# Kernel tuning notes

Measured on AMD Instinct MI355X. Metric: run time of the kernel, lower is better.

## Reference

```python
import jax, jax.numpy as jnp
import numpy as np

S = 2048      # total tokens
DIM = 1024    # model dim
H = 16        # attention heads
DH = 64       # head dim
BOT = 256     # bottleneck dim
NIMG = 4      # images (equal size)
L = S // NIMG # tokens per image
K = 256       # sparse_k
IH = 4        # indexer heads
ID = 16       # indexer head dim
MAXREL = 64   # hardcoded in module
NBUCK = 2 * MAXREL + 1
GH = IH * 2   # gate MLP hidden (expansion=2)


def setup_inputs() -> dict:
    key = jax.random.key(0)
    ks = jax.random.split(key, 16)
    r = lambda i, sh, s=0.02: jax.random.normal(ks[i], sh, jnp.float32) * s
    return dict(
        hidden_states=jax.random.normal(ks[0], (S, DIM), jnp.float32),
        patch_coords=jax.random.randint(ks[1], (S, 2), 0, 64, dtype=jnp.int32),
        cu_seqlens=jnp.arange(NIMG + 1, dtype=jnp.int32) * L,
        rotary_pos_emb=jax.random.uniform(ks[2], (S, DH // 2), jnp.float32) * 3.0,
        Wq_idx=r(3, (2 * IH * ID, DIM)),
        Wk_idx=r(4, (2 * IH * ID, DIM)),
        W1g=r(5, (GH, IH)), b1g=jnp.zeros((GH,), jnp.float32),
        W2g=r(6, (IH, GH)), b2g=jnp.zeros((IH,), jnp.float32),
        rpe_table=r(7, (NBUCK, IH)),
        Wqkv_d=r(8, (BOT, DIM)), bqkv_d=jnp.zeros((BOT,), jnp.float32),
        Wqkv_u=r(9, (3 * DIM, BOT)), bqkv_u=jnp.zeros((3 * DIM,), jnp.float32),
        Wp_d=r(10, (BOT, DIM)), bp_d=jnp.zeros((BOT,), jnp.float32),
        Wp_u=r(11, (DIM, BOT)), bp_u=jnp.zeros((DIM,), jnp.float32),
        scaler=jnp.ones((1,), jnp.float32),
    )


def _rotate_half(x):
    x1, x2 = jnp.split(x, 2, axis=-1)
    return jnp.concatenate([-x2, x1], axis=-1)


def reference(hidden_states, patch_coords, cu_seqlens, rotary_pos_emb,
              Wq_idx, Wk_idx, W1g, b1g, W2g, b2g, rpe_table,
              Wqkv_d, bqkv_d, Wqkv_u, bqkv_u, Wp_d, bp_d, Wp_u, bp_u, scaler):
    n = cu_seqlens.shape[0] - 1            # images (equal size L)
    Li = hidden_states.shape[0] // n
    neg = jnp.finfo(hidden_states.dtype).min

    # QKV via low-rank bottleneck
    qkv = (hidden_states @ Wqkv_d.T + bqkv_d) @ Wqkv_u.T + bqkv_u  # [S, 3*DIM]
    qkv = qkv.reshape(S, 3, H, DH)
    q, k, v = qkv[:, 0], qkv[:, 1], qkv[:, 2]                      # [S, H, DH]

    # vision RoPE (emb = cat(rpe, rpe))
    emb = jnp.concatenate([rotary_pos_emb, rotary_pos_emb], axis=-1)  # [S, DH]
    cos = jnp.cos(emb)[:, None, :]
    sin = jnpp if False else jnp.sin(emb)[:, None, :]
    q = q * cos + _rotate_half(q) * sin
    k = k * cos + _rotate_half(k) * sin

    # ---- interaction indexer, vmapped over equal-size images ----
    xs = hidden_states.reshape(n, Li, DIM)
    pos = patch_coords[:, 1].reshape(n, Li).astype(jnp.float32)
    qI = (xs @ Wq_idx.T).reshape(n, Li, 2 * IH, ID)
    kI = (xs @ Wk_idx.T).reshape(n, Li, 2 * IH, ID)
    dot = jnp.einsum('nqhd,nkhd->nqkh', qI, kI)                    # [n, L, L, 2*IH]
    data_in, gate_in = dot[..., :IH], dot[..., IH:]
    rel = jnp.clip(pos[:, :, None] - pos[:, None, :], -MAXREL, MAXREL)
    bucket = (rel + MAXREL).astype(jnp.int32)                      # [n, L, L]
    rpe = rpe_table[bucket]                                        # [n, L, L, IH]
    relu_scores = jax.nn.relu(data_in + rpe)
    g = jax.nn.sigmoid(jax.nn.relu((gate_in + rpe) @ W1g.T + b1g) @ W2g.T + b2g)
    index_scores = (relu_scores * g).sum(-1)                       # [n, L, L]

    # top-k sparse mask (0 at selected keys, -inf-ish elsewhere)
    _, topk_idx = jax.lax.top_k(index_scores, K)                   # [n, L, K]
    ni = jnp.arange(n)[:, None, None]
    ri = jnp.arange(Li)[None, :, None]
    mask_local = jnp.full((n, Li, Li), neg, hidden_states.dtype).at[ni, ri, topk_idx].set(0.0)

    # block-diagonal full mask
    mask = jnp.full((S, S), neg, hidden_states.dtype)
    for i in range(n):
        mask = mask.at[i * Li:(i + 1) * Li, i * Li:(i + 1) * Li].set(mask_local[i])

    # dense SDPA with additive mask
    att = jnp.einsum('qhd,khd->hqk', q, k) / jnp.sqrt(jnp.float32(DH)).astype(q.dtype)
    att = att + mask[None]
    p = jax.nn.softmax(att, axis=-1)
    out = jnp.einsum('hqk,khd->qhd', p, v).reshape(S, H * DH)

    final = (out @ Wp_d.T + bp_d) @ Wp_u.T + bp_u
    return final * scaler
```

## Files before the change

kernel.cpp:

```cpp
#include <hip/hip_runtime.h>
#include <hip/hip_bf16.h>

#define S_    2048
#define DIM_  1024
#define H_    16
#define DH_   64
#define BOT_  256
#define NIMG_ 4
#define LI_   512
#define K_    256
#define IH_   4
#define ID_   16
#define MAXREL_ 64
#define NBUCK_ 129
#define GH_   8
#define IDH2_ 128

typedef short bf16x8 __attribute__((ext_vector_type(8)));
typedef float f32x4  __attribute__((ext_vector_type(4)));

__device__ __forceinline__ unsigned short f2bf(float x) {
    unsigned u = __float_as_uint(x);
    return (unsigned short)((u + 0x7fffu + ((u >> 16) & 1u)) >> 16);
}
__device__ __forceinline__ float bf2f(unsigned short h) {
    return __uint_as_float(((unsigned)h) << 16);
}

#define OFF_W1_    2097152
#define OFF_WQ_    2359296
#define OFF_WK_    2490368
#define OFF_WQKVU_ 2621440
#define OFF_WPD_   3407872
#define OFF_WPU_   3670016
#define NSPLIT_    3932160

__global__ __launch_bounds__(256) void split_all_kernel(
    const float* __restrict__ hid, const float* __restrict__ wqd,
    const float* __restrict__ wq,  const float* __restrict__ wk,
    const float* __restrict__ wqu, const float* __restrict__ wpd,
    const float* __restrict__ wpu,
    unsigned short* __restrict__ hi, unsigned short* __restrict__ lo)
{
    long e = ((long)blockIdx.x * 256 + threadIdx.x) * 4;
    if (e >= NSPLIT_) return;
    const float* src; long off;
    if (e < OFF_W1_)         { src = hid; off = 0; }
    else if (e < OFF_WQ_)    { src = wqd; off = OFF_W1_; }
    else if (e < OFF_WK_)    { src = wq;  off = OFF_WQ_; }
    else if (e < OFF_WQKVU_) { src = wk;  off = OFF_WK_; }
    else if (e < OFF_WPD_)   { src = wqu; off = OFF_WQKVU_; }
    else if (e < OFF_WPU_)   { src = wpd; off = OFF_WPD_; }
    else                     { src = wpu; off = OFF_WPU_; }
    float4 v = *(const float4*)(src + (e - off));
    ushort4 h, l;
    h.x = f2bf(v.x); l.x = f2bf(v.x - bf2f(h.x));
    h.y = f2bf(v.y); l.y = f2bf(v.y - bf2f(h.y));
    h.z = f2bf(v.z); l.z = f2bf(v.z - bf2f(h.z));
    h.w = f2bf(v.w); l.w = f2bf(v.w - bf2f(h.w));
    *(ushort4*)&hi[e] = h;
    *(ushort4*)&lo[e] = l;
}

__global__ __launch_bounds__(256) void gemm_bf16x3(
    const unsigned short* __restrict__ Ah, const unsigned short* __restrict__ Al,
    const unsigned short* __restrict__ Bh, const unsigned short* __restrict__ Bl,
    const float* __restrict__ bias, const float* __restrict__ scale_ptr,
    float* __restrict__ Cf, int M, int N, int Kd)
{
    __shared__ unsigned short sAh[128 * 40], sAl[128 * 40];
    __shared__ unsigned short sBh[64 * 40],  sBl[64 * 40];
    int tid = threadIdx.x;
    int lane = tid & 63, wv = tid >> 6;
    int wr = wv >> 1, wc = wv & 1;
    int row0 = blockIdx.y * 128, col0 = blockIdx.x * 64;

    f32x4 acc[4][2];
#pragma unroll
    for (int i = 0; i < 4; i++)
#pragma unroll
        for (int j = 0; j < 2; j++) acc[i][j] = (f32x4){0.f, 0.f, 0.f, 0.f};

    int ar = tid >> 1, ac = (tid & 1) * 16;
    int br = tid >> 2, bc = (tid & 3) * 8;
    const unsigned short* gAh = Ah + (size_t)(row0 + ar) * Kd + ac;
    const unsigned short* gAl = Al + (size_t)(row0 + ar) * Kd + ac;
    const unsigned short* gBh = Bh + (size_t)(col0 + br) * Kd + bc;
    const unsigned short* gBl = Bl + (size_t)(col0 + br) * Kd + bc;
    int am = lane & 15, qk = (lane >> 4) * 8;

    for (int k0 = 0; k0 < Kd; k0 += 32) {
        __syncthreads();
        *(float4*)&sAh[ar * 40 + ac]     = *(const float4*)(gAh + k0);
        *(float4*)&sAh[ar * 40 + ac + 8] = *(const float4*)(gAh + k0 + 8);
        *(float4*)&sAl[ar * 40 + ac]     = *(const float4*)(gAl + k0);
        *(float4*)&sAl[ar * 40 + ac + 8] = *(const float4*)(gAl + k0 + 8);
        *(float4*)&sBh[br * 40 + bc]     = *(const float4*)(gBh + k0);
        *(float4*)&sBl[br * 40 + bc]     = *(const float4*)(gBl + k0);
        __syncthreads();

        bf16x8 ah[4], al[4], bh[2], bl[2];
#pragma unroll
        for (int rt = 0; rt < 4; rt++) {
            int r = wr * 64 + rt * 16 + am;
            ah[rt] = *(const bf16x8*)&sAh[r * 40 + qk];
            al[rt] = *(const bf16x8*)&sAl[r * 40 + qk];
        }
#pragma unroll
        for (int ct = 0; ct < 2; ct++) {
            int c = wc * 32 + ct * 16 + am;
            bh[ct] = *(const bf16x8*)&sBh[c * 40 + qk];
            bl[ct] = *(const bf16x8*)&sBl[c * 40 + qk];
        }
#pragma unroll
        for (int rt = 0; rt < 4; rt++)
#pragma unroll
            for (int ct = 0; ct < 2; ct++) {
                acc[rt][ct] = __builtin_amdgcn_mfma_f32_16x16x32_bf16(ah[rt], bh[ct], acc[rt][ct], 0, 0, 0);
                acc[rt][ct] = __builtin_amdgcn_mfma_f32_16x16x32_bf16(ah[rt], bl[ct], acc[rt][ct], 0, 0, 0);
                acc[rt][ct] = __builtin_amdgcn_mfma_f32_16x16x32_bf16(al[rt], bh[ct], acc[rt][ct], 0, 0, 0);
            }
    }

    float scl = scale_ptr ? *scale_ptr : 1.0f;
    int rq = (lane >> 4) * 4;
#pragma unroll
    for (int rt = 0; rt < 4; rt++)
#pragma unroll
        for (int ct = 0; ct < 2; ct++) {
            int col = col0 + wc * 32 + ct * 16 + am;
            float bz = bias ? bias[col] : 0.0f;
#pragma unroll
            for (int rg = 0; rg < 4; rg++) {
                int row = row0 + wr * 64 + rt * 16 + rq + rg;
                Cf[(size_t)row * N + col] = (acc[rt][ct][rg] + bz) * scl;
            }
        }
}

__global__ __launch_bounds__(256) void gemm64_bf16x3(
    const unsigned short* __restrict__ Ah, const unsigned short* __restrict__ Al,
    const unsigned short* __restrict__ Bh, const unsigned short* __restrict__ Bl,
    const float* __restrict__ bias_lo, const float* __restrict__ bias_hi,
    float* __restrict__ Cf, unsigned short* __restrict__ Chi,
    unsigned short* __restrict__ Clo, int M, int N, int Kd, int split_col)
{
    __shared__ unsigned short sAh[64 * 40], sAl[64 * 40];
    __shared__ unsigned short sBh[64 * 40], sBl[64 * 40];
    int tid = threadIdx.x;
    int lane = tid & 63, wv = tid >> 6;
    int wr = wv >> 1, wc = wv & 1;
    int row0 = blockIdx.y * 64, col0 = blockIdx.x * 64;

    f32x4 acc[2][2];
#pragma unroll
    for (int i = 0; i < 2; i++)
#pragma unroll
        for (int j = 0; j < 2; j++) acc[i][j] = (f32x4){0.f, 0.f, 0.f, 0.f};

    int sr = tid >> 2, sc = (tid & 3) * 8;
    const unsigned short* gAh = Ah + (size_t)(row0 + sr) * Kd + sc;
    const unsigned short* gAl = Al + (size_t)(row0 + sr) * Kd + sc;
    const unsigned short* gBh = Bh + (size_t)(col0 + sr) * Kd + sc;
    const unsigned short* gBl = Bl + (size_t)(col0 + sr) * Kd + sc;
    int am = lane & 15, qk = (lane >> 4) * 8;

    for (int k0 = 0; k0 < Kd; k0 += 32) {
        __syncthreads();
        *(float4*)&sAh[sr * 40 + sc] = *(const float4*)(gAh + k0);
        *(float4*)&sAl[sr * 40 + sc] = *(const float4*)(gAl + k0);
        *(float4*)&sBh[sr * 40 + sc] = *(const float4*)(gBh + k0);
        *(float4*)&sBl[sr * 40 + sc] = *(const float4*)(gBl + k0);
        __syncthreads();

        bf16x8 ah[2], al[2], bh[2], bl[2];
#pragma unroll
        for (int rt = 0; rt < 2; rt++) {
            int r = wr * 32 + rt * 16 + am;
            ah[rt] = *(const bf16x8*)&sAh[r * 40 + qk];
            al[rt] = *(const bf16x8*)&sAl[r * 40 + qk];
        }
#pragma unroll
        for (int ct = 0; ct < 2; ct++) {
            int c = wc * 32 + ct * 16 + am;
            bh[ct] = *(const bf16x8*)&sBh[c * 40 + qk];
            bl[ct] = *(const bf16x8*)&sBl[c * 40 + qk];
        }
#pragma unroll
        for (int rt = 0; rt < 2; rt++)
#pragma unroll
            for (int ct = 0; ct < 2; ct++) {
                acc[rt][ct] = __builtin_amdgcn_mfma_f32_16x16x32_bf16(ah[rt], bh[ct], acc[rt][ct], 0, 0, 0);
                acc[rt][ct] = __builtin_amdgcn_mfma_f32_16x16x32_bf16(ah[rt], bl[ct], acc[rt][ct], 0, 0, 0);
                acc[rt][ct] = __builtin_amdgcn_mfma_f32_16x16x32_bf16(al[rt], bh[ct], acc[rt][ct], 0, 0, 0);
            }
    }

    int rq = (lane >> 4) * 4;
#pragma unroll
    for (int rt = 0; rt < 2; rt++)
#pragma unroll
        for (int ct = 0; ct < 2; ct++) {
            int col = col0 + wc * 32 + ct * 16 + am;
#pragma unroll
            for (int rg = 0; rg < 4; rg++) {
                int row = row0 + wr * 32 + rt * 16 + rq + rg;
                float v = acc[rt][ct][rg];
                if (col < split_col) {
                    if (bias_lo) v += bias_lo[col];
                    size_t idx = (size_t)row * split_col + col;
                    unsigned short hh = f2bf(v);
                    Chi[idx] = hh;
                    Clo[idx] = f2bf(v - bf2f(hh));
                } else {
                    if (bias_hi) v += bias_hi[col - split_col];
                    Cf[(size_t)row * (N - split_col) + col - split_col] = v;
                }
            }
        }
}

__global__ __launch_bounds__(256) void rope_kernel(
    float* __restrict__ qkv, const float* __restrict__ rope)
{
    int idx = blockIdx.x * blockDim.x + threadIdx.x;
    if (idx >= S_ * H_ * 32) return;
    int d = idx & 31;
    int h = (idx >> 5) & (H_ - 1);
    int s = idx >> 9;
    float r = rope[s * 32 + d];
    float c = cosf(r), sn = sinf(r);
    size_t base = (size_t)s * 3072 + h * 64 + d;
    float q1 = qkv[base], q2 = qkv[base + 32];
    qkv[base]      = q1 * c - q2 * sn;
    qkv[base + 32] = q2 * c + q1 * sn;
    float k1 = qkv[base + 1024], k2 = qkv[base + 1024 + 32];
    qkv[base + 1024]      = k1 * c - k2 * sn;
    qkv[base + 1024 + 32] = k2 * c + k1 * sn;
}

__global__ __launch_bounds__(256) void score_topk_kernel(
    const float* __restrict__ qIk,
    const int* __restrict__ coords, const float* __restrict__ rpe_table,
    const float* __restrict__ W1g, const float* __restrict__ b1g,
    const float* __restrict__ W2g, const float* __restrict__ b2g,
    unsigned* __restrict__ selmask)
{
    __shared__ float skI[64][132];
    __shared__ float sqI2[4][IDH2_];
    __shared__ unsigned skeys[4][LI_];
    __shared__ int shist[4][256];
    __shared__ float srpe[NBUCK_ * IH_];
    __shared__ float sW1[GH_ * IH_], sb1[GH_], sW2[IH_ * GH_], sb2[IH_];

    int tid  = threadIdx.x;
    int lane = tid & 63;
    int wv   = tid >> 6;
    int row  = blockIdx.x * 4 + wv;
    int n    = (blockIdx.x * 4) >> 9;

    for (int i = tid; i < NBUCK_ * IH_; i += 256) srpe[i] = rpe_table[i];
    if (tid < 32) sW1[tid] = W1g[tid];
    else if (tid < 64) sW2[tid - 32] = W2g[tid - 32];
    else if (tid < 72) sb1[tid - 64] = b1g[tid - 64];
    else if (tid < 76) sb2[tid - 72] = b2g[tid - 72];
    for (int i = tid; i < 4 * IDH2_; i += 256)
        sqI2[i >> 7][i & 127] =
            qIk[(size_t)(blockIdx.x * 4 + (i >> 7)) * 256 + (i & 127)];
    int pq = coords[row * 2 + 1];

    for (int kt = 0; kt < 8; kt++) {
        __syncthreads();
        {
            int r  = tid >> 2;
            int d0 = (tid & 3) * 32;
            const float* src = qIk + (size_t)(n * LI_ + kt * 64 + r) * 256 + 128 + d0;
#pragma unroll
            for (int j = 0; j < 8; j++)
                *(float4*)&skI[r][d0 + j * 4] = *(const float4*)(src + j * 4);
        }
        __syncthreads();

        int kloc = lane;
        int kg   = kt * 64 + kloc;
        const float* sq = &sqI2[wv][0];
        float dh[8];
#pragma unroll
        for (int hh = 0; hh < 8; hh++) {
            float acc = 0.0f;
#pragma unroll
            for (int d = 0; d < 16; d += 4) {
                float4 kv = *(const float4*)&skI[kloc][hh * 16 + d];
                acc += sq[hh * 16 + d + 0] * kv.x + sq[hh * 16 + d + 1] * kv.y +
                       sq[hh * 16 + d + 2] * kv.z + sq[hh * 16 + d + 3] * kv.w;
            }
            dh[hh] = acc;
        }
        int pk = coords[(n * LI_ + kg) * 2 + 1];
        int rel = pq - pk;
        rel = rel < -MAXREL_ ? -MAXREL_ : (rel > MAXREL_ ? MAXREL_ : rel);
        const float* rp = srpe + (rel + MAXREL_) * IH_;
        float t1[GH_];
#pragma unroll
        for (int g = 0; g < GH_; g++) t1[g] = sb1[g];
#pragma unroll
        for (int j = 0; j < IH_; j++) {
            float gate = dh[IH_ + j] + rp[j];
#pragma unroll
            for (int g = 0; g < GH_; g++) t1[g] += gate * sW1[g * IH_ + j];
        }
#pragma unroll
        for (int g = 0; g < GH_; g++) t1[g] = fmaxf(t1[g], 0.0f);
        float score = 0.0f;
#pragma unroll
        for (int j = 0; j < IH_; j++) {
            float t2 = sb2[j];
#pragma unroll
            for (int g = 0; g < GH_; g++) t2 += t1[g] * sW2[j * GH_ + g];
            float sg = 1.0f / (1.0f + expf(-t2));
            float rs = fmaxf(dh[j] + rp[j], 0.0f);
            score += rs * sg;
        }
        unsigned bits = __float_as_uint(score);
        skeys[wv][kg] = (bits & 0x80000000u) ? ~bits : (bits | 0x80000000u);
    }
    __syncthreads();

    unsigned pref = 0u;
    int kcur = K_;
    const unsigned himask[4] = {0u, 0xFF000000u, 0xFFFF0000u, 0xFFFFFF00u};
#pragma unroll
    for (int pass = 0; pass < 4; pass++) {
        int shift = 24 - pass * 8;
        unsigned hm = himask[pass];
        *(int4*)&shist[wv][4 * lane] = make_int4(0, 0, 0, 0);
        __syncthreads();
#pragma unroll
        for (int c = 0; c < 8; c++) {
            unsigned key = skeys[wv][c * 64 + lane];
            if ((key & hm) == pref) atomicAdd(&shist[wv][(key >> shift) & 255], 1);
        }
        __syncthreads();
        int4 b4 = *(const int4*)&shist[wv][4 * lane];
        int b[4] = {b4.x, b4.y, b4.z, b4.w};
        int t = b[0] + b[1] + b[2] + b[3];
        int Ssum = t;
#pragma unroll
        for (int off = 1; off < 64; off <<= 1) {
            int u = __shfl_down(Ssum, off, 64);
            if (lane + off < 64) Ssum += u;
        }
        int E = Ssum - t;
        int cs[5];
        cs[4] = E;
        cs[3] = b[3] + E;
        cs[2] = b[2] + cs[3];
        cs[1] = b[1] + cs[2];
        cs[0] = b[0] + cs[1];
        bool found = false;
        unsigned cpref = 0u; int ck = 0;
#pragma unroll
        for (int j = 0; j < 4; j++) {
            if (!found && cs[j] >= kcur && cs[j + 1] < kcur) {
                found = true;
                cpref = pref | ((unsigned)(4 * lane + j) << shift);
                ck = kcur - cs[j + 1];
            }
        }
        unsigned long long bm = __ballot(found);
        int src = __ffsll((long long)bm) - 1;
        pref = (unsigned)__shfl((int)cpref, src, 64);
        kcur = __shfl(ck, src, 64);
        __syncthreads();
    }
    unsigned Tu = pref;

    unsigned long long bg[8], be[8];
#pragma unroll
    for (int c = 0; c < 8; c++) {
        unsigned key = skeys[wv][c * 64 + lane];
        bg[c] = __ballot(key > Tu);
        be[c] = __ballot(key == Tu);
    }
    if (lane < 16) {
        int total_gt = 0;
#pragma unroll
        for (int c = 0; c < 8; c++) total_gt += __popcll(bg[c]);
        int base = 0;
#pragma unroll
        for (int c = 0; c < 8; c++) {
            if (2 * c < lane)     base += __popc((unsigned)be[c]);
            if (2 * c + 1 < lane) base += __popc((unsigned)(be[c] >> 32));
        }
        unsigned gw = (unsigned)(bg[lane >> 1] >> (32 * (lane & 1)));
        unsigned ew = (unsigned)(be[lane >> 1] >> (32 * (lane & 1)));
        int ne = K_ - total_gt - base;
        int pc = __popc(ew);
        int m = ne < 0 ? 0 : (ne > pc ? pc : ne);
        while (pc > m) { ew ^= (1u << (31 - __clz(ew))); pc--; }
        selmask[(size_t)row * 16 + lane] = gw | ew;
    }
}

__global__ __launch_bounds__(256) void attn_kernel(
    const float* __restrict__ qkv, const unsigned* __restrict__ selmask,
    unsigned short* __restrict__ outh, unsigned short* __restrict__ outl)
{
    __shared__ float Qs[64][68];
    __shared__ float KPs[64][68];
    __shared__ float Vs[64][68];
    __shared__ unsigned Ms[64][16];

    int b  = blockIdx.x;
    int qt = b >> 6;
    int nh = b & 63;
    int h  = nh & 15;
    int n  = nh >> 4;
    int tid = threadIdx.x;
    int tx = tid & 15, ty = tid >> 4;
    int q0 = n * LI_ + qt * 64;

    for (int i = tid; i < 64 * 16; i += 256)
        Ms[i >> 4][i & 15] = selmask[(size_t)(q0 + (i >> 4)) * 16 + (i & 15)];

#pragma unroll
    for (int m = 0; m < 4; m++) {
        int r = (tid >> 4) + m * 16;
        int c = tid & 15;
        float4 v = *(const float4*)(qkv + (size_t)(q0 + r) * 3072 + h * 64 + c * 4);
        Qs[c * 4 + 0][r] = v.x * 0.125f;
        Qs[c * 4 + 1][r] = v.y * 0.125f;
        Qs[c * 4 + 2][r] = v.z * 0.125f;
        Qs[c * 4 + 3][r] = v.w * 0.125f;
    }

    float o[4][4] = {};
    float rs[4] = {};

    for (int kt = 0; kt < 8; kt++) {
        __syncthreads();
#pragma unroll
        for (int m = 0; m < 4; m++) {
            int r = (tid >> 4) + m * 16;
            int c = tid & 15;
            size_t krow = (size_t)(n * LI_ + kt * 64 + r) * 3072 + h * 64;
            float4 kv = *(const float4*)(qkv + krow + 1024 + c * 4);
            KPs[c * 4 + 0][r] = kv.x;
            KPs[c * 4 + 1][r] = kv.y;
            KPs[c * 4 + 2][r] = kv.z;
            KPs[c * 4 + 3][r] = kv.w;
            float4 vv = *(const float4*)(qkv + krow + 2048 + c * 4);
            *(float4*)&Vs[r][c * 4] = vv;
        }
        __syncthreads();

        float s[4][4] = {};
#pragma unroll 8
        for (int d = 0; d < 64; d++) {
            float4 a4 = *(const float4*)&Qs[d][ty * 4];
            float4 b4 = *(const float4*)&KPs[d][tx * 4];
            float a[4] = {a4.x, a4.y, a4.z, a4.w};
            float bb[4] = {b4.x, b4.y, b4.z, b4.w};
#pragma unroll
            for (int i = 0; i < 4; i++)
#pragma unroll
                for (int j = 0; j < 4; j++)
                    s[i][j] += a[i] * bb[j];
        }

        int kbase = kt * 64 + tx * 4;
        int wi = kbase >> 5;
        int bit0 = kbase & 31;
        float pcol[4][4];
#pragma unroll
        for (int i = 0; i < 4; i++) {
            unsigned mw = Ms[ty * 4 + i][wi];
#pragma unroll
            for (int j = 0; j < 4; j++) {
                float p = ((mw >> (bit0 + j)) & 1u) ? __expf(s[i][j]) : 0.0f;
                rs[i] += p;
                pcol[j][i] = p;
            }
        }
        __syncthreads();

#pragma unroll
        for (int j = 0; j < 4; j++)
            *(float4*)&KPs[tx * 4 + j][ty * 4] =
                make_float4(pcol[j][0], pcol[j][1], pcol[j][2], pcol[j][3]);
        __syncthreads();

#pragma unroll 4
        for (int k = 0; k < 64; k++) {
            float4 p4 = *(const float4*)&KPs[k][ty * 4];
            float4 v4 = *(const float4*)&Vs[k][tx * 4];
            o[0][0] += p4.x * v4.x; o[0][1] += p4.x * v4.y;
            o[0][2] += p4.x * v4.z; o[0][3] += p4.x * v4.w;
            o[1][0] += p4.y * v4.x; o[1][1] += p4.y * v4.y;
            o[1][2] += p4.y * v4.z; o[1][3] += p4.y * v4.w;
            o[2][0] += p4.z * v4.x; o[2][1] += p4.z * v4.y;
            o[2][2] += p4.z * v4.z; o[2][3] += p4.z * v4.w;
            o[3][0] += p4.w * v4.x; o[3][1] += p4.w * v4.y;
            o[3][2] += p4.w * v4.z; o[3][3] += p4.w * v4.w;
        }
    }

#pragma unroll
    for (int i = 0; i < 4; i++) {
#pragma unroll
        for (int off = 1; off < 16; off <<= 1)
            rs[i] += __shfl_xor(rs[i], off, 64);
    }

#pragma unroll
    for (int i = 0; i < 4; i++) {
        float inv = 1.0f / rs[i];
        size_t ob = (size_t)(q0 + ty * 4 + i) * 1024 + h * 64 + tx * 4;
        ushort4 hv, lv;
        float v0 = o[i][0] * inv; hv.x = f2bf(v0); lv.x = f2bf(v0 - bf2f(hv.x));
        float v1 = o[i][1] * inv; hv.y = f2bf(v1); lv.y = f2bf(v1 - bf2f(hv.y));
        float v2 = o[i][2] * inv; hv.z = f2bf(v2); lv.z = f2bf(v2 - bf2f(hv.z));
        float v3 = o[i][3] * inv; hv.w = f2bf(v3); lv.w = f2bf(v3 - bf2f(hv.w));
        *(ushort4*)&outh[ob] = hv;
        *(ushort4*)&outl[ob] = lv;
    }
}

extern "C" void kernel_launch(void* const* d_in, const int* in_sizes, int n_in,
                              void* d_out, int out_size, void* d_ws, size_t ws_size,
                              hipStream_t stream)
{
    const float* hidden  = (const float*)d_in[0];
    const int*   coords  = (const int*)d_in[1];
    const float* rope    = (const float*)d_in[3];
    const float* Wq_idx  = (const float*)d_in[4];
    const float* Wk_idx  = (const float*)d_in[5];
    const float* W1g     = (const float*)d_in[6];
    const float* b1g     = (const float*)d_in[7];
    const float* W2g     = (const float*)d_in[8];
    const float* b2g     = (const float*)d_in[9];
    const float* rpe     = (const float*)d_in[10];
    const float* Wqkv_d  = (const float*)d_in[11];
    const float* bqkv_d  = (const float*)d_in[12];
    const float* Wqkv_u  = (const float*)d_in[13];
    const float* bqkv_u  = (const float*)d_in[14];
    const float* Wp_d    = (const float*)d_in[15];
    const float* bp_d    = (const float*)d_in[16];
    const float* Wp_u    = (const float*)d_in[17];
    const float* bp_u    = (const float*)d_in[18];
    const float* scaler  = (const float*)d_in[19];
    float* out = (float*)d_out;

    unsigned short* sp_hi  = (unsigned short*)d_ws;
    unsigned short* sp_lo  = sp_hi + NSPLIT_;
    unsigned short* mid_hi = sp_lo + NSPLIT_;
    unsigned short* mid_lo = mid_hi + (size_t)S_ * BOT_;
    float* qkv = (float*)(mid_lo + (size_t)S_ * BOT_);
    float* qIk = qkv + (size_t)S_ * 3 * DIM_;
    unsigned* selmask = (unsigned*)(qIk + (size_t)S_ * 256);

    split_all_kernel<<<(NSPLIT_ / 4 + 255) / 256, 256, 0, stream>>>(
        hidden, Wqkv_d, Wq_idx, Wk_idx, Wqkv_u, Wp_d, Wp_u, sp_hi, sp_lo);

    gemm64_bf16x3<<<dim3(512 / 64, S_ / 64), 256, 0, stream>>>(
        sp_hi, sp_lo, sp_hi + OFF_W1_, sp_lo + OFF_W1_,
        bqkv_d, nullptr, qIk, mid_hi, mid_lo, S_, 512, DIM_, 256);

    gemm_bf16x3<<<dim3(3 * DIM_ / 64, S_ / 128), 256, 0, stream>>>(
        mid_hi, mid_lo, sp_hi + OFF_WQKVU_, sp_lo + OFF_WQKVU_,
        bqkv_u, nullptr, qkv, S_, 3 * DIM_, BOT_);

    rope_kernel<<<(S_ * H_ * 32) / 256, 256, 0, stream>>>(qkv, rope);

    score_topk_kernel<<<S_ / 4, 256, 0, stream>>>(
        qIk, coords, rpe, W1g, b1g, W2g, b2g, selmask);

    attn_kernel<<<NIMG_ * H_ * 8, 256, 0, stream>>>(qkv, selmask, sp_hi, sp_lo);

    gemm64_bf16x3<<<dim3(BOT_ / 64, S_ / 64), 256, 0, stream>>>(
        sp_hi, sp_lo, sp_hi + OFF_WPD_, sp_lo + OFF_WPD_,
        bp_d, nullptr, nullptr, mid_hi, mid_lo, S_, BOT_, DIM_, BOT_);

    gemm_bf16x3<<<dim3(DIM_ / 64, S_ / 128), 256, 0, stream>>>(
        mid_hi, mid_lo, sp_hi + OFF_WPU_, sp_lo + OFF_WPU_,
        bp_u, scaler, out, S_, DIM_, BOT_);
}
```

Measured before the change: 290.3 us.

## Rewrite attention kernel to use bf16x3 split MFMA for QK and PV

Replaces the fp32 scalar FMA inner loops of the attention kernel with MFMA 16x16x32 bf16 instructions. Q, K, V and P are each split into high and low bf16 parts and combined with three MFMAs to approximate fp32 precision. V is stored transposed in shared memory, and the probability tile is rewritten in split form for the PV product. This trades the per-tile conversion work and strided V loads for matrix-core throughput on what was an ALU-bound block.

```diff
diff --git a/kernel.cpp b/kernel.cpp
--- a/kernel.cpp
+++ b/kernel.cpp
@@ -406,9 +406,9 @@
     const float* __restrict__ qkv, const unsigned* __restrict__ selmask,
     unsigned short* __restrict__ outh, unsigned short* __restrict__ outl)
 {
-    __shared__ float Qs[64][68];
-    __shared__ float KPs[64][68];
-    __shared__ float Vs[64][68];
+    __shared__ unsigned short Qh[64 * 72],  Ql[64 * 72];
+    __shared__ unsigned short KPh[64 * 72], KPl[64 * 72];
+    __shared__ unsigned short VTh[64 * 72], VTl[64 * 72];
     __shared__ unsigned Ms[64][16];
 
     int b  = blockIdx.x;
@@ -417,112 +417,160 @@
     int h  = nh & 15;
     int n  = nh >> 4;
     int tid = threadIdx.x;
-    int tx = tid & 15, ty = tid >> 4;
+    int lane = tid & 63, w = tid >> 6;
+    int lane15 = lane & 15, quad = lane >> 4;
     int q0 = n * LI_ + qt * 64;
 
     for (int i = tid; i < 64 * 16; i += 256)
         Ms[i >> 4][i & 15] = selmask[(size_t)(q0 + (i >> 4)) * 16 + (i & 15)];
 
-#pragma unroll
-    for (int m = 0; m < 4; m++) {
-        int r = (tid >> 4) + m * 16;
-        int c = tid & 15;
-        float4 v = *(const float4*)(qkv + (size_t)(q0 + r) * 3072 + h * 64 + c * 4);
-        Qs[c * 4 + 0][r] = v.x * 0.125f;
-        Qs[c * 4 + 1][r] = v.y * 0.125f;
-        Qs[c * 4 + 2][r] = v.z * 0.125f;
-        Qs[c * 4 + 3][r] = v.w * 0.125f;
-    }
-
-    float o[4][4] = {};
-    float rs[4] = {};
+    {
+        int r = tid >> 2, c0 = (tid & 3) * 16;
+        const float* src = qkv + (size_t)(q0 + r) * 3072 + h * 64 + c0;
+        unsigned short hb[16], lb[16];
+#pragma unroll
+        for (int j = 0; j < 16; j += 4) {
+            float4 v = *(const float4*)(src + j);
+            float f[4] = {v.x * 0.125f, v.y * 0.125f, v.z * 0.125f, v.w * 0.125f};
+#pragma unroll
+            for (int t = 0; t < 4; t++) {
+                unsigned short hh = f2bf(f[t]);
+                hb[j + t] = hh;
+                lb[j + t] = f2bf(f[t] - bf2f(hh));
+            }
+        }
+        *(uint4*)&Qh[r * 72 + c0]     = *(uint4*)&hb[0];
+        *(uint4*)&Qh[r * 72 + c0 + 8] = *(uint4*)&hb[8];
+        *(uint4*)&Ql[r * 72 + c0]     = *(uint4*)&lb[0];
+        *(uint4*)&Ql[r * 72 + c0 + 8] = *(uint4*)&lb[8];
+    }
+
+    f32x4 o_acc[4];
+#pragma unroll
+    for (int i = 0; i < 4; i++) o_acc[i] = (f32x4){0.f, 0.f, 0.f, 0.f};
+    float rsum[4] = {};
 
     for (int kt = 0; kt < 8; kt++) {
         __syncthreads();
-#pragma unroll
-        for (int m = 0; m < 4; m++) {
-            int r = (tid >> 4) + m * 16;
-            int c = tid & 15;
-            size_t krow = (size_t)(n * LI_ + kt * 64 + r) * 3072 + h * 64;
-            float4 kv = *(const float4*)(qkv + krow + 1024 + c * 4);
-            KPs[c * 4 + 0][r] = kv.x;
-            KPs[c * 4 + 1][r] = kv.y;
-            KPs[c * 4 + 2][r] = kv.z;
-            KPs[c * 4 + 3][r] = kv.w;
-            float4 vv = *(const float4*)(qkv + krow + 2048 + c * 4);
-            *(float4*)&Vs[r][c * 4] = vv;
-        }
-        __syncthreads();
-
-        float s[4][4] = {};
-#pragma unroll 8
-        for (int d = 0; d < 64; d++) {
-            float4 a4 = *(const float4*)&Qs[d][ty * 4];
-            float4 b4 = *(const float4*)&KPs[d][tx * 4];
-            float a[4] = {a4.x, a4.y, a4.z, a4.w};
-            float bb[4] = {b4.x, b4.y, b4.z, b4.w};
-#pragma unroll
-            for (int i = 0; i < 4; i++)
-#pragma unroll
-                for (int j = 0; j < 4; j++)
-                    s[i][j] += a[i] * bb[j];
-        }
-
-        int kbase = kt * 64 + tx * 4;
-        int wi = kbase >> 5;
-        int bit0 = kbase & 31;
-        float pcol[4][4];
-#pragma unroll
-        for (int i = 0; i < 4; i++) {
-            unsigned mw = Ms[ty * 4 + i][wi];
-#pragma unroll
-            for (int j = 0; j < 4; j++) {
-                float p = ((mw >> (bit0 + j)) & 1u) ? __expf(s[i][j]) : 0.0f;
-                rs[i] += p;
-                pcol[j][i] = p;
-            }
-        }
-        __syncthreads();
-
-#pragma unroll
-        for (int j = 0; j < 4; j++)
-            *(float4*)&KPs[tx * 4 + j][ty * 4] =
-                make_float4(pcol[j][0], pcol[j][1], pcol[j][2], pcol[j][3]);
-        __syncthreads();
-
-#pragma unroll 4
-        for (int k = 0; k < 64; k++) {
-            float4 p4 = *(const float4*)&KPs[k][ty * 4];
-            float4 v4 = *(const float4*)&Vs[k][tx * 4];
-            o[0][0] += p4.x * v4.x; o[0][1] += p4.x * v4.y;
-            o[0][2] += p4.x * v4.z; o[0][3] += p4.x * v4.w;
-            o[1][0] += p4.y * v4.x; o[1][1] += p4.y * v4.y;
-            o[1][2] += p4.y * v4.z; o[1][3] += p4.y * v4.w;
-            o[2][0] += p4.z * v4.x; o[2][1] += p4.z * v4.y;
-            o[2][2] += p4.z * v4.z; o[2][3] += p4.z * v4.w;
-            o[3][0] += p4.w * v4.x; o[3][1] += p4.w * v4.y;
-            o[3][2] += p4.w * v4.z; o[3][3] += p4.w * v4.w;
-        }
-    }
-
-#pragma unroll
-    for (int i = 0; i < 4; i++) {
-#pragma unroll
-        for (int off = 1; off < 16; off <<= 1)
-            rs[i] += __shfl_xor(rs[i], off, 64);
-    }
-
-#pragma unroll
-    for (int i = 0; i < 4; i++) {
-        float inv = 1.0f / rs[i];
-        size_t ob = (size_t)(q0 + ty * 4 + i) * 1024 + h * 64 + tx * 4;
-        ushort4 hv, lv;
-        float v0 = o[i][0] * inv; hv.x = f2bf(v0); lv.x = f2bf(v0 - bf2f(hv.x));
-        float v1 = o[i][1] * inv; hv.y = f2bf(v1); lv.y = f2bf(v1 - bf2f(hv.y));
-        float v2 = o[i][2] * inv; hv.z = f2bf(v2); lv.z = f2bf(v2 - bf2f(hv.z));
-        float v3 = o[i][3] * inv; hv.w = f2bf(v3); lv.w = f2bf(v3 - bf2f(hv.w));
-        *(ushort4*)&outh[ob] = hv;
-        *(ushort4*)&outl[ob] = lv;
+        {
+            int r = tid >> 2, c0 = (tid & 3) * 16;
+            const float* src = qkv + (size_t)(n * LI_ + kt * 64 + r) * 3072 + 1024 + h * 64 + c0;
+            unsigned short hb[16], lb[16];
+#pragma unroll
+            for (int j = 0; j < 16; j += 4) {
+                float4 v = *(const float4*)(src + j);
+                float f[4] = {v.x, v.y, v.z, v.w};
+#pragma unroll
+                for (int t = 0; t < 4; t++) {
+                    unsigned short hh = f2bf(f[t]);
+                    hb[j + t] = hh;
+                    lb[j + t] = f2bf(f[t] - bf2f(hh));
+                }
+            }
+            *(uint4*)&KPh[r * 72 + c0]     = *(uint4*)&hb[0];
+            *(uint4*)&KPh[r * 72 + c0 + 8] = *(uint4*)&hb[8];
+            *(uint4*)&KPl[r * 72 + c0]     = *(uint4*)&lb[0];
+            *(uint4*)&KPl[r * 72 + c0 + 8] = *(uint4*)&lb[8];
+        }
+        {
+            int d = lane;
+            int k0 = w * 16;
+            const float* src = qkv + (size_t)(n * LI_ + kt * 64 + k0) * 3072 + 2048 + h * 64 + d;
+            unsigned short hb[16], lb[16];
+#pragma unroll
+            for (int j = 0; j < 16; j++) {
+                float f = src[(size_t)j * 3072];
+                unsigned short hh = f2bf(f);
+                hb[j] = hh;
+                lb[j] = f2bf(f - bf2f(hh));
+            }
+            *(uint4*)&VTh[d * 72 + k0]     = *(uint4*)&hb[0];
+            *(uint4*)&VTh[d * 72 + k0 + 8] = *(uint4*)&hb[8];
+            *(uint4*)&VTl[d * 72 + k0]     = *(uint4*)&lb[0];
+            *(uint4*)&VTl[d * 72 + k0 + 8] = *(uint4*)&lb[8];
+        }
+        __syncthreads();
+
+        f32x4 s_acc[4];
+#pragma unroll
+        for (int nt = 0; nt < 4; nt++) s_acc[nt] = (f32x4){0.f, 0.f, 0.f, 0.f};
+        {
+            bf16x8 qfh[2], qfl[2];
+#pragma unroll
+            for (int ks = 0; ks < 2; ks++) {
+                qfh[ks] = *(const bf16x8*)&Qh[(16 * w + lane15) * 72 + ks * 32 + quad * 8];
+                qfl[ks] = *(const bf16x8*)&Ql[(16 * w + lane15) * 72 + ks * 32 + quad * 8];
+            }
+#pragma unroll
+            for (int nt = 0; nt < 4; nt++) {
+#pragma unroll
+                for (int ks = 0; ks < 2; ks++) {
+                    bf16x8 kfh = *(const bf16x8*)&KPh[(16 * nt + lane15) * 72 + ks * 32 + quad * 8];
+                    bf16x8 kfl = *(const bf16x8*)&KPl[(16 * nt + lane15) * 72 + ks * 32 + quad * 8];
+                    s_acc[nt] = __builtin_amdgcn_mfma_f32_16x16x32_bf16(qfh[ks], kfh, s_acc[nt], 0, 0, 0);
+                    s_acc[nt] = __builtin_amdgcn_mfma_f32_16x16x32_bf16(qfh[ks], kfl, s_acc[nt], 0, 0, 0);
+                    s_acc[nt] = __builtin_amdgcn_mfma_f32_16x16x32_bf16(qfl[ks], kfh, s_acc[nt], 0, 0, 0);
+                }
+            }
+        }
+        __syncthreads();
+
+#pragma unroll
+        for (int nt = 0; nt < 4; nt++) {
+            int kb = kt * 64 + nt * 16 + lane15;
+            int wi = kb >> 5, bit = kb & 31;
+#pragma unroll
+            for (int reg = 0; reg < 4; reg++) {
+                int qloc = 16 * w + quad * 4 + reg;
+                unsigned mw = Ms[qloc][wi];
+                float p = ((mw >> bit) & 1u) ? __expf(s_acc[nt][reg]) : 0.0f;
+                rsum[reg] += p;
+                unsigned short ph = f2bf(p);
+                KPh[qloc * 72 + nt * 16 + lane15] = ph;
+                KPl[qloc * 72 + nt * 16 + lane15] = f2bf(p - bf2f(ph));
+            }
+        }
+        __syncthreads();
+
+        {
+            bf16x8 pfh[2], pfl[2];
+#pragma unroll
+            for (int ks = 0; ks < 2; ks++) {
+                pfh[ks] = *(const bf16x8*)&KPh[(16 * w + lane15) * 72 + ks * 32 + quad * 8];
+                pfl[ks] = *(const bf16x8*)&KPl[(16 * w + lane15) * 72 + ks * 32 + quad * 8];
+            }
+#pragma unroll
+            for (int dt = 0; dt < 4; dt++) {
+#pragma unroll
+                for (int ks = 0; ks < 2; ks++) {
+                    bf16x8 vfh = *(const bf16x8*)&VTh[(16 * dt + lane15) * 72 + ks * 32 + quad * 8];
+                    bf16x8 vfl = *(const bf16x8*)&VTl[(16 * dt + lane15) * 72 + ks * 32 + quad * 8];
+                    o_acc[dt] = __builtin_amdgcn_mfma_f32_16x16x32_bf16(pfh[ks], vfh, o_acc[dt], 0, 0, 0);
+                    o_acc[dt] = __builtin_amdgcn_mfma_f32_16x16x32_bf16(pfh[ks], vfl, o_acc[dt], 0, 0, 0);
+                    o_acc[dt] = __builtin_amdgcn_mfma_f32_16x16x32_bf16(pfl[ks], vfh, o_acc[dt], 0, 0, 0);
+                }
+            }
+        }
+    }
+
+#pragma unroll
+    for (int reg = 0; reg < 4; reg++) {
+        rsum[reg] += __shfl_xor(rsum[reg], 1, 64);
+        rsum[reg] += __shfl_xor(rsum[reg], 2, 64);
+        rsum[reg] += __shfl_xor(rsum[reg], 4, 64);
+        rsum[reg] += __shfl_xor(rsum[reg], 8, 64);
+    }
+
+#pragma unroll
+    for (int dt = 0; dt < 4; dt++) {
+#pragma unroll
+        for (int reg = 0; reg < 4; reg++) {
+            float v = o_acc[dt][reg] / rsum[reg];
+            size_t ob = (size_t)(q0 + 16 * w + quad * 4 + reg) * 1024 + h * 64 + 16 * dt + lane15;
+            unsigned short hh = f2bf(v);
+            outh[ob] = hh;
+            outl[ob] = f2bf(v - bf2f(hh));
+        }
     }
 }
 
```

Result: faster. 255.3 us (-12.1%).
